# Optimization experiments

Hardware: AMD Instinct MI355X
Metric: run time of the kernel (lower is better)

Reference implementation:

```python
import jax, jax.numpy as jnp
import numpy as np

B, N, C = 8, 2000, 512
H, W, SR = 8, 5, 2          # num_heads, window_size, sr_ratio
LN_EPS = 1e-5


def setup_inputs() -> dict:
    key = jax.random.key(0)
    ks = jax.random.split(key, 6)
    s = lambda k, shape: jax.random.normal(k, shape, jnp.float32) * 0.02
    return {
        "x": jax.random.normal(ks[0], (B, N, C), jnp.float32),
        "Wq": s(ks[1], (C, C)),      "bq": jnp.zeros((C,), jnp.float32),
        "Wkv": s(ks[2], (2 * C, C)), "bkv": jnp.zeros((2 * C,), jnp.float32),
        "Wc": s(ks[3], (C, C)),      "bc": jnp.zeros((C,), jnp.float32),
        "ln_g": jnp.ones((C,), jnp.float32), "ln_b": jnp.zeros((C,), jnp.float32),
        "Wp": s(ks[4], (C, C)),      "bp": jnp.zeros((C,), jnp.float32),
    }


def reference(x, Wq, bq, Wkv, bkv, Wc, bc, ln_g, ln_b, Wp, bp):
    Bx, Nx, Cx = x.shape
    hd = Cx // H
    scale = hd ** (-0.5)
    G = Nx // W          # number of local windows
    M = Nx // SR         # pooled length

    # q: [B,H,N,hd]
    q = (x @ Wq.T + bq).reshape(Bx, Nx, H, hd).transpose(0, 2, 1, 3)

    # local kv: [B,G,W,2,H,hd] -> k_l/v_l [B,H,G,W,hd]
    kv = (x @ Wkv.T + bkv).reshape(Bx, G, W, 2, H, hd)
    k_l = kv[:, :, :, 0].transpose(0, 3, 1, 2, 4)
    v_l = kv[:, :, :, 1].transpose(0, 3, 1, 2, 4)

    # windowed local scores: group q into windows, einsum within window
    # (equivalent to torch's repeat_interleave + per-query matmul, but no blowup)
    qw = q.reshape(Bx, H, G, W, hd)
    attn_local = jnp.einsum('bhgqd,bhgkd->bhgqk', qw, k_l).reshape(Bx, H, Nx, W) * scale

    # pooled branch: AvgPool1d(sr) -> 1x1 conv -> LayerNorm -> GELU(exact)
    xp = x.reshape(Bx, M, SR, Cx).mean(axis=2)
    xp = xp @ Wc.T + bc
    mu = xp.mean(-1, keepdims=True)
    var = xp.var(-1, keepdims=True)
    xp = (xp - mu) / jnp.sqrt(var + LN_EPS) * ln_g + ln_b
    xp = jax.nn.gelu(xp, approximate=False)

    kvp = (xp @ Wkv.T + bkv).reshape(Bx, M, 2, H, hd)
    k_p = kvp[:, :, 0].transpose(0, 2, 1, 3)   # [B,H,M,hd]
    v_p = kvp[:, :, 1].transpose(0, 2, 1, 3)

    attn_pool = jnp.einsum('bhnd,bhmd->bhnm', q, k_p) * scale  # [B,H,N,M]

    # joint softmax over local window + pooled keys
    attn = jax.nn.softmax(jnp.concatenate([attn_local, attn_pool], axis=-1), axis=-1)
    a_l = attn[..., :W].reshape(Bx, H, G, W, W)
    a_p = attn[..., W:]

    x_l = jnp.einsum('bhgqk,bhgkd->bhgqd', a_l, v_l).reshape(Bx, H, Nx, hd)
    x_p = jnp.einsum('bhnm,bhmd->bhnd', a_p, v_p)

    out = (x_l + x_p).transpose(0, 2, 1, 3).reshape(Bx, Nx, Cx)
    return out @ Wp.T + bp
```

## Files before the change

### kernel.cpp

```cpp
#include <hip/hip_runtime.h>
#include <hip/hip_bf16.h>
#include <math.h>

#define B_   8
#define N_   2000
#define C_   512
#define H_   8
#define W_   5
#define SR_  2
#define M_   1000
#define HD_  64
#define KK_  512
#define RP_  8192
#define NPAD_ 16384
#define LN_EPS_ 1e-5f
#define SCALE_  0.125f
#define QSC_    0.18033688011112042f

#define TQ_   128
#define NCH_  16
#define KSTR2 72

typedef __attribute__((ext_vector_type(8))) short bf16x8;
typedef __attribute__((ext_vector_type(4))) short short4v;
typedef __attribute__((ext_vector_type(4))) float f32x4;
typedef __attribute__((ext_vector_type(16))) float f32x16;
#define MFMA16(a,b,c) __builtin_amdgcn_mfma_f32_16x16x32_bf16(a,b,c,0,0,0)
#define MFMA32(a,b,c) __builtin_amdgcn_mfma_f32_32x32x16_bf16(a,b,c,0,0,0)

__device__ __forceinline__ short f2bf(float f) {
  unsigned u = __float_as_uint(f);
  u += 0x7FFFu + ((u >> 16) & 1u);
  return (short)(u >> 16);
}
__device__ __forceinline__ uint2 pack4bf(float4 v) {
  unsigned a = ((unsigned)(unsigned short)f2bf(v.x)) | (((unsigned)(unsigned short)f2bf(v.y)) << 16);
  unsigned b = ((unsigned)(unsigned short)f2bf(v.z)) | (((unsigned)(unsigned short)f2bf(v.w)) << 16);
  return make_uint2(a, b);
}

__device__ __forceinline__ float wave_sum(float v) {
#pragma unroll
  for (int o = 32; o > 0; o >>= 1) v += __shfl_xor(v, o);
  return v;
}

__device__ __forceinline__ void gl_lds16(const void* g, void* l) {
  __builtin_amdgcn_global_load_lds(
      (const __attribute__((address_space(1))) void*)g,
      (__attribute__((address_space(3))) void*)l, 16, 0, 0);
}

__global__ __launch_bounds__(256) void cvt_bf16(const float* __restrict__ src,
                                                short* __restrict__ dst, int n8) {
  int i = blockIdx.x * 256 + threadIdx.x;
  if (i >= n8) return;
  float4 a = reinterpret_cast<const float4*>(src)[i * 2];
  float4 b = reinterpret_cast<const float4*>(src)[i * 2 + 1];
  uint2 pa = pack4bf(a), pb = pack4bf(b);
  reinterpret_cast<uint4*>(dst)[i] = make_uint4(pa.x, pa.y, pb.x, pb.y);
}

__global__ __launch_bounds__(256) void cvt_pool(const float* __restrict__ X,
                                                short* __restrict__ Xb,
                                                short* __restrict__ Xp) {
  int idx = blockIdx.x * 256 + threadIdx.x;
  const int total = B_ * M_ * (C_ / 8);
  if (idx >= total) return;
  int row = idx / (C_ / 8);
  int c8  = idx % (C_ / 8);
  int b = row / M_, m = row % M_;
  size_t r0 = ((size_t)b * N_ + 2 * m) * C_ + c8 * 8;
  size_t r1 = r0 + C_;
  float4 a0 = *(const float4*)(X + r0), a1 = *(const float4*)(X + r0 + 4);
  float4 b0 = *(const float4*)(X + r1), b1 = *(const float4*)(X + r1 + 4);
  uint2 pa0 = pack4bf(a0), pa1 = pack4bf(a1);
  uint2 pb0 = pack4bf(b0), pb1 = pack4bf(b1);
  *(uint4*)(Xb + r0) = make_uint4(pa0.x, pa0.y, pa1.x, pa1.y);
  *(uint4*)(Xb + r1) = make_uint4(pb0.x, pb0.y, pb1.x, pb1.y);
  float4 s0, s1;
  s0.x = 0.5f * (a0.x + b0.x); s0.y = 0.5f * (a0.y + b0.y);
  s0.z = 0.5f * (a0.z + b0.z); s0.w = 0.5f * (a0.w + b0.w);
  s1.x = 0.5f * (a1.x + b1.x); s1.y = 0.5f * (a1.y + b1.y);
  s1.z = 0.5f * (a1.z + b1.z); s1.w = 0.5f * (a1.w + b1.w);
  uint2 q0 = pack4bf(s0), q1 = pack4bf(s1);
  *(uint4*)(Xp + (size_t)row * C_ + c8 * 8) = make_uint4(q0.x, q0.y, q1.x, q1.y);
}

template<int OUT_BF16>
__global__ __launch_bounds__(256) void gemm_mfma(const short* __restrict__ A,
                                                 const short* __restrict__ Bm,
                                                 const float* __restrict__ bias,
                                                 void* __restrict__ Yv,
                                                 int O, float oscale) {
  __shared__ short As[128 * 32];
  __shared__ short Bs[128 * 32];
  const int tid  = threadIdx.x;
  const int w    = tid >> 6;
  const int lane = tid & 63;
  const int g    = lane >> 4;
  const int c0   = lane & 15;
  const int wr   = w >> 1;
  const int wc   = w & 1;
  const long r0 = (long)blockIdx.y * 128;
  const long o0 = (long)blockIdx.x * 128;
  const int srow = lane >> 2;
  const int scol = (lane & 3) * 8;

  f32x4 acc[4][4];
#pragma unroll
  for (int m = 0; m < 4; ++m)
#pragma unroll
    for (int n = 0; n < 4; ++n) acc[m][n] = (f32x4){0.f, 0.f, 0.f, 0.f};

  for (int kk = 0; kk < 16; ++kk) {
    __syncthreads();
#pragma unroll
    for (int i = 0; i < 2; ++i) {
      int arow = i * 64 + w * 16;
      gl_lds16(A  + (r0 + arow + srow) * KK_ + kk * 32 + scol, &As[arow * 32]);
      gl_lds16(Bm + (o0 + arow + srow) * KK_ + kk * 32 + scol, &Bs[arow * 32]);
    }
    __syncthreads();
    bf16x8 a[4], b[4];
#pragma unroll
    for (int m = 0; m < 4; ++m) a[m] = *(const bf16x8*)&As[(wr * 64 + m * 16 + c0) * 32 + g * 8];
#pragma unroll
    for (int n = 0; n < 4; ++n) b[n] = *(const bf16x8*)&Bs[(wc * 64 + n * 16 + c0) * 32 + g * 8];
#pragma unroll
    for (int m = 0; m < 4; ++m)
#pragma unroll
      for (int n = 0; n < 4; ++n) acc[m][n] = MFMA16(a[m], b[n], acc[m][n]);
  }

#pragma unroll
  for (int m = 0; m < 4; ++m) {
    long row = r0 + wr * 64 + m * 16 + g * 4;
#pragma unroll
    for (int n = 0; n < 4; ++n) {
      long col = o0 + wc * 64 + n * 16 + c0;
      float bv = bias[col];
#pragma unroll
      for (int r = 0; r < 4; ++r) {
        float v = (acc[m][n][r] + bv) * oscale;
        if (OUT_BF16) ((short*)Yv)[(row + r) * O + col] = f2bf(v);
        else          ((float*)Yv)[(row + r) * O + col] = v;
      }
    }
  }
}

__global__ __launch_bounds__(256) void gemm_qkv(const short* __restrict__ A,
                                                const short* __restrict__ Bm,
                                                const float* __restrict__ bq,
                                                const float* __restrict__ bkv,
                                                short* __restrict__ Yq,
                                                short* __restrict__ Ykv) {
  __shared__ short As[128 * 32];
  __shared__ short Bs[128 * 32];
  const int tid  = threadIdx.x;
  const int w    = tid >> 6;
  const int lane = tid & 63;
  const int g    = lane >> 4;
  const int c0   = lane & 15;
  const int wr   = w >> 1;
  const int wc   = w & 1;
  const long r0 = (long)blockIdx.y * 128;
  const long o0 = (long)blockIdx.x * 128;
  const int srow = lane >> 2;
  const int scol = (lane & 3) * 8;

  f32x4 acc[4][4];
#pragma unroll
  for (int m = 0; m < 4; ++m)
#pragma unroll
    for (int n = 0; n < 4; ++n) acc[m][n] = (f32x4){0.f, 0.f, 0.f, 0.f};

  for (int kk = 0; kk < 16; ++kk) {
    __syncthreads();
#pragma unroll
    for (int i = 0; i < 2; ++i) {
      int arow = i * 64 + w * 16;
      gl_lds16(A  + (r0 + arow + srow) * KK_ + kk * 32 + scol, &As[arow * 32]);
      gl_lds16(Bm + (o0 + arow + srow) * KK_ + kk * 32 + scol, &Bs[arow * 32]);
    }
    __syncthreads();
    bf16x8 a[4], b[4];
#pragma unroll
    for (int m = 0; m < 4; ++m) a[m] = *(const bf16x8*)&As[(wr * 64 + m * 16 + c0) * 32 + g * 8];
#pragma unroll
    for (int n = 0; n < 4; ++n) b[n] = *(const bf16x8*)&Bs[(wc * 64 + n * 16 + c0) * 32 + g * 8];
#pragma unroll
    for (int m = 0; m < 4; ++m)
#pragma unroll
      for (int n = 0; n < 4; ++n) acc[m][n] = MFMA16(a[m], b[n], acc[m][n]);
  }

  const bool isq = (blockIdx.x < 4);
#pragma unroll
  for (int m = 0; m < 4; ++m) {
    long row = r0 + wr * 64 + m * 16 + g * 4;
#pragma unroll
    for (int n = 0; n < 4; ++n) {
      long col = o0 + wc * 64 + n * 16 + c0;
      if (isq) {
        float bv = bq[col];
#pragma unroll
        for (int r = 0; r < 4; ++r)
          Yq[(row + r) * 512 + col] = f2bf((acc[m][n][r] + bv) * QSC_);
      } else {
        long ck = col - 512;
        float bv = bkv[ck];
#pragma unroll
        for (int r = 0; r < 4; ++r)
          Ykv[(row + r) * 1024 + ck] = f2bf(acc[m][n][r] + bv);
      }
    }
  }
}

__global__ __launch_bounds__(256) void ln_gelu(const float* __restrict__ Xc,
                                               short* __restrict__ Xo,
                                               const float* __restrict__ gam,
                                               const float* __restrict__ bet) {
  const int row = blockIdx.x;
  const float* p = Xc + (size_t)row * C_;
  const int t = threadIdx.x;
  float v0 = p[t], v1 = p[t + 256];
  float s  = wave_sum(v0 + v1);
  float ss = wave_sum(v0 * v0 + v1 * v1);
  __shared__ float rs[4], rss[4];
  const int w = t >> 6, lane = t & 63;
  if (lane == 0) { rs[w] = s; rss[w] = ss; }
  __syncthreads();
  float ts  = rs[0] + rs[1] + rs[2] + rs[3];
  float tss = rss[0] + rss[1] + rss[2] + rss[3];
  float mean = ts * (1.0f / C_);
  float var  = tss * (1.0f / C_) - mean * mean;
  float rstd = rsqrtf(var + LN_EPS_);
  float u0 = (v0 - mean) * rstd * gam[t]       + bet[t];
  float u1 = (v1 - mean) * rstd * gam[t + 256] + bet[t + 256];
  Xo[(size_t)row * C_ + t]       = f2bf(u0 * 0.5f * (1.0f + erff(u0 * 0.70710678118654752f)));
  Xo[(size_t)row * C_ + t + 256] = f2bf(u1 * 0.5f * (1.0f + erff(u1 * 0.70710678118654752f)));
}

template<int MODE>
__device__ __forceinline__ void tile32(const short* Ksb, const short* Vtb,
                                       const bf16x8 qf[4],
                                       float& m_c, float& l_c, f32x16* o,
                                       int c, int hi, int koff)
{
  f32x16 sblk[2];
  __builtin_amdgcn_s_setprio(1);
#pragma unroll
  for (int kb = 0; kb < 2; ++kb) {
    f32x16 acc = {};
#pragma unroll
    for (int sl = 0; sl < 4; ++sl) {
      bf16x8 kf = *(const bf16x8*)&Ksb[(kb*32 + c)*KSTR2 + sl*16 + hi*8];
      acc = MFMA32(kf, qf[sl], acc);
    }
    sblk[kb] = acc;
  }
  __builtin_amdgcn_s_setprio(0);

  if (MODE == 1) {
#pragma unroll
    for (int kb = 0; kb < 2; ++kb)
#pragma unroll
      for (int r = 0; r < 16; ++r) {
        int ku = koff + kb*32 + ((r & 3) + 8*(r >> 2));
        if ((unsigned)ku >= 5u) sblk[kb][r] = -3.0e38f;
      }
  }
  if (MODE == 2) {
#pragma unroll
    for (int r = 4; r < 16; ++r) sblk[1][r] = -3.0e38f;
  }

  float t16[16];
#pragma unroll
  for (int r = 0; r < 16; ++r) t16[r] = fmaxf(sblk[0][r], sblk[1][r]);
#pragma unroll
  for (int st = 8; st > 0; st >>= 1)
#pragma unroll
    for (int r = 0; r < st; ++r) t16[r] = fmaxf(t16[r], t16[r + st]);
  float pmax = fmaxf(t16[0], __shfl_xor(t16[0], 32));

  if (!__all(pmax - m_c <= 8.0f)) {
    float mn = fmaxf(m_c, pmax);
    float al = exp2f(m_c - mn);
    m_c = mn;
    l_c *= al;
    o[0] *= al;
    o[1] *= al;
  }

  float rs4[4] = {0.f, 0.f, 0.f, 0.f};
  int dw[2][8];
#pragma unroll
  for (int kb = 0; kb < 2; ++kb)
#pragma unroll
    for (int i = 0; i < 8; ++i) {
      float p0 = exp2f(sblk[kb][2*i]     - m_c);
      float p1 = exp2f(sblk[kb][2*i + 1] - m_c);
      rs4[i & 3] += p0 + p1;
      int d;
      asm("v_cvt_pk_bf16_f32 %0, %1, %2" : "=v"(d) : "v"(p0), "v"(p1));
      dw[kb][i] = d;
    }
  float rs = (rs4[0] + rs4[1]) + (rs4[2] + rs4[3]);
  rs += __shfl_xor(rs, 32);
  l_c += rs;

  bf16x8 pfrag[2][2];
#pragma unroll
  for (int kb = 0; kb < 2; ++kb)
#pragma unroll
    for (int kp = 0; kp < 2; ++kp) {
      union { int i[4]; bf16x8 v; } u;
      u.i[0] = dw[kb][kp*4 + 0];
      u.i[1] = dw[kb][kp*4 + 1];
      u.i[2] = dw[kb][kp*4 + 2];
      u.i[3] = dw[kb][kp*4 + 3];
      pfrag[kb][kp] = u.v;
    }

  __builtin_amdgcn_s_setprio(1);
#pragma unroll
  for (int db = 0; db < 2; ++db)
#pragma unroll
    for (int kb = 0; kb < 2; ++kb)
#pragma unroll
      for (int kp = 0; kp < 2; ++kp) {
        bf16x8 vf = *(const bf16x8*)&Vtb[(db*32 + c)*KSTR2 + kb*32 + kp*16 + hi*8];
        o[db] = MFMA32(vf, pfrag[kb][kp], o[db]);
      }
  __builtin_amdgcn_s_setprio(0);
}

__global__ __launch_bounds__(256, 3) void attn_mfma32(const short* __restrict__ Q,
                                                      const short* __restrict__ KV,
                                                      const short* __restrict__ KVP,
                                                      short* __restrict__ Oa) {
  __shared__ __align__(16) short Ks[2][64 * KSTR2];
  __shared__ __align__(16) short Vt[2][64 * KSTR2];

  const int bid   = blockIdx.x;
  const int bh    = bid & 63;
  const int chunk = bid >> 6;
  const int b     = bh >> 3;
  const int h     = bh & 7;
  const int n0    = chunk * TQ_;
  const int tid  = threadIdx.x;
  const int wq   = tid >> 6;
  const int lane = tid & 63;
  const int c    = lane & 31;
  const int hi   = lane >> 5;

  const int qabs = n0 + wq * 32 + c;
  const size_t qrow = (size_t)(b * N_ + qabs) * C_ + h * HD_;
  bf16x8 qf[4];
#pragma unroll
  for (int sl = 0; sl < 4; ++sl) qf[sl] = *(const bf16x8*)(Q + qrow + sl*16 + hi*8);

  const int qlo = (qabs / 5) * 5;
  const int klo = (n0 / 5) * 5;
  const int wlo = ((n0 + wq*32) / 5) * 5;
  const int whi = ((n0 + wq*32 + 31) / 5) * 5 + 5;

  const int kkey = tid >> 3, kdq = tid & 7;
  const int vkp  = tid & 31, vdq = (tid >> 5) & 7;
  const int svkp = (vkp & ~6) | ((vkp & 2) << 1) | ((vkp & 4) >> 1);
  bf16x8 rk0, rk1, rv0, rv1;

  auto issue = [&](const short* pb_) {
    rk0 = *(const bf16x8*)(pb_ + (size_t)kkey        * (2*C_) + h*HD_ + kdq*8);
    rk1 = *(const bf16x8*)(pb_ + (size_t)(kkey + 32) * (2*C_) + h*HD_ + kdq*8);
    rv0 = *(const bf16x8*)(pb_ + (size_t)(2*vkp)     * (2*C_) + C_ + h*HD_ + vdq*8);
    rv1 = *(const bf16x8*)(pb_ + (size_t)(2*vkp + 1) * (2*C_) + C_ + h*HD_ + vdq*8);
  };
  auto write = [&](int buf) {
    *(bf16x8*)&Ks[buf][kkey * KSTR2 + kdq * 8]        = rk0;
    *(bf16x8*)&Ks[buf][(kkey + 32) * KSTR2 + kdq * 8] = rk1;
#pragma unroll
    for (int e = 0; e < 8; ++e) {
      unsigned wv = ((unsigned)(unsigned short)rv0[e]) | (((unsigned)(unsigned short)rv1[e]) << 16);
      *(unsigned*)&Vt[buf][(vdq*8 + e) * KSTR2 + 2*svkp] = wv;
    }
  };

  const short* kvloc = KV  + (size_t)(b * N_ + klo) * (2*C_);
  const short* kvp_b = KVP + (size_t)(b * M_)       * (2*C_);

  float m_c = 0.f, l_c = 0.f;
  f32x16 o[2];
  o[0] = (f32x16){}; o[1] = (f32x16){};

  issue(kvloc);
  write(0);
  __syncthreads();
  int cur = 0;

#pragma unroll 1
  for (int t = 0; t < 3; ++t) {
    const short* nxt = (t < 2) ? kvloc + (size_t)(t + 1) * 64 * (2*C_) : kvp_b;
    issue(nxt);
    const int base = klo + t * 64;
    if (base < whi && base + 64 > wlo)
      tile32<1>(Ks[cur], Vt[cur], qf, m_c, l_c, o, c, hi, base + 4*hi - qlo);
    write(cur ^ 1);
    __syncthreads();
    cur ^= 1;
  }
#pragma unroll 1
  for (int t = 0; t < 15; ++t) {
    issue(kvp_b + (size_t)(t + 1) * 64 * (2*C_));
    tile32<0>(Ks[cur], Vt[cur], qf, m_c, l_c, o, c, hi, 0);
    write(cur ^ 1);
    __syncthreads();
    cur ^= 1;
  }
  tile32<2>(Ks[cur], Vt[cur], qf, m_c, l_c, o, c, hi, 0);

  if (qabs < N_) {
    float inv = 1.0f / l_c;
    short* orow = Oa + ((size_t)(b * N_ + qabs)) * C_ + h * HD_;
#pragma unroll
    for (int db = 0; db < 2; ++db)
#pragma unroll
      for (int rq = 0; rq < 4; ++rq) {
        short4v sv;
#pragma unroll
        for (int i = 0; i < 4; ++i) sv[i] = f2bf(o[db][rq*4 + i] * inv);
        *(short4v*)(orow + db*32 + rq*8 + 4*hi) = sv;
      }
  }
}

extern "C" void kernel_launch(void* const* d_in, const int* in_sizes, int n_in,
                              void* d_out, int out_size, void* d_ws, size_t ws_size,
                              hipStream_t stream) {
  const float* x   = (const float*)d_in[0];
  const float* Wq  = (const float*)d_in[1];
  const float* bq  = (const float*)d_in[2];
  const float* Wkv = (const float*)d_in[3];
  const float* bkv = (const float*)d_in[4];
  const float* Wc  = (const float*)d_in[5];
  const float* bc  = (const float*)d_in[6];
  const float* lng = (const float*)d_in[7];
  const float* lnb = (const float*)d_in[8];
  const float* Wp  = (const float*)d_in[9];
  const float* bp  = (const float*)d_in[10];
  float* out = (float*)d_out;

  float* xc   = (float*)d_ws;
  short* sb   = (short*)(xc + (size_t)RP_ * 512);
  short* xb    = sb;
  short* qb    = xb   + (size_t)16000 * 512;
  short* kvb   = qb   + (size_t)NPAD_ * 512;
  short* xpb   = kvb  + (size_t)NPAD_ * 1024;
  short* xcb   = xpb  + (size_t)RP_ * 512;
  short* kvpb  = xcb  + (size_t)RP_ * 512;
  short* aoutb = kvpb + (size_t)RP_ * 1024;
  short* Wqkvb = aoutb + (size_t)16000 * 512;
  short* Wcb   = Wqkvb + (size_t)1536 * 512;
  short* Wpb   = Wcb  + (size_t)512 * 512;

  dim3 blk(256);

  cvt_pool<<<dim3((B_*M_*(C_/8) + 255)/256), blk, 0, stream>>>(x, xb, xpb);
  cvt_bf16<<<dim3((512*512/8  + 255)/256), blk, 0, stream>>>(Wq,  Wqkvb,             512*512/8);
  cvt_bf16<<<dim3((1024*512/8 + 255)/256), blk, 0, stream>>>(Wkv, Wqkvb + 512*512,   1024*512/8);
  cvt_bf16<<<dim3((512*512/8  + 255)/256), blk, 0, stream>>>(Wc,  Wcb,  512*512/8);
  cvt_bf16<<<dim3((512*512/8  + 255)/256), blk, 0, stream>>>(Wp,  Wpb,  512*512/8);

  gemm_mfma<0><<<dim3(C_/128, RP_/128), blk, 0, stream>>>(xpb, Wcb, bc, xc, C_, 1.0f);
  ln_gelu<<<dim3(B_ * M_), blk, 0, stream>>>(xc, xcb, lng, lnb);
  gemm_mfma<1><<<dim3((2*C_)/128, RP_/128), blk, 0, stream>>>(xcb, Wqkvb + 512*512, bkv, kvpb, 2*C_, 1.0f);

  gemm_qkv<<<dim3(1536/128, 16000/128), blk, 0, stream>>>(xb, Wqkvb, bq, bkv, qb, kvb);

  attn_mfma32<<<dim3(64 * NCH_), blk, 0, stream>>>(qb, kvb, kvpb, aoutb);

  gemm_mfma<0><<<dim3(C_/128, 16000/128), blk, 0, stream>>>(aoutb, Wpb, bp, out, C_, 1.0f);
}
```

Measured before the change: 193.4 us.

## Double-buffer LDS tiles in both GEMM kernels and raise attention occupancy bound

Both the generic MFMA GEMM and the fused QKV GEMM now keep two LDS buffers per operand. The next K-slice is loaded with global-to-LDS copies while MFMAs run on the current slice, which leaves one barrier per iteration instead of two. The attention kernel's launch bounds are raised from 3 to 4 waves-per-EU minimum, which may force register spills in exchange for higher occupancy. LDS use per GEMM block doubles.

```diff
diff --git a/kernel.cpp b/kernel.cpp
--- a/kernel.cpp
+++ b/kernel.cpp
@@ -93,8 +93,8 @@
                                                  const float* __restrict__ bias,
                                                  void* __restrict__ Yv,
                                                  int O, float oscale) {
-  __shared__ short As[128 * 32];
-  __shared__ short Bs[128 * 32];
+  __shared__ short As[2][128 * 32];
+  __shared__ short Bs[2][128 * 32];
   const int tid  = threadIdx.x;
   const int w    = tid >> 6;
   const int lane = tid & 63;
@@ -107,30 +107,39 @@
   const int srow = lane >> 2;
   const int scol = (lane & 3) * 8;
 
-  f32x4 acc[4][4];
-#pragma unroll
-  for (int m = 0; m < 4; ++m)
-#pragma unroll
-    for (int n = 0; n < 4; ++n) acc[m][n] = (f32x4){0.f, 0.f, 0.f, 0.f};
-
-  for (int kk = 0; kk < 16; ++kk) {
-    __syncthreads();
+  auto stage = [&](int buf, int kk) {
 #pragma unroll
     for (int i = 0; i < 2; ++i) {
       int arow = i * 64 + w * 16;
-      gl_lds16(A  + (r0 + arow + srow) * KK_ + kk * 32 + scol, &As[arow * 32]);
-      gl_lds16(Bm + (o0 + arow + srow) * KK_ + kk * 32 + scol, &Bs[arow * 32]);
-    }
+      gl_lds16(A  + (r0 + arow + srow) * KK_ + kk * 32 + scol, &As[buf][arow * 32]);
+      gl_lds16(Bm + (o0 + arow + srow) * KK_ + kk * 32 + scol, &Bs[buf][arow * 32]);
+    }
+  };
+
+  f32x4 acc[4][4];
+#pragma unroll
+  for (int m = 0; m < 4; ++m)
+#pragma unroll
+    for (int n = 0; n < 4; ++n) acc[m][n] = (f32x4){0.f, 0.f, 0.f, 0.f};
+
+  stage(0, 0);
+  __syncthreads();
+  int cur = 0;
+
+#pragma unroll 1
+  for (int kk = 0; kk < 16; ++kk) {
+    if (kk < 15) stage(cur ^ 1, kk + 1);
+    bf16x8 a[4], b[4];
+#pragma unroll
+    for (int m = 0; m < 4; ++m) a[m] = *(const bf16x8*)&As[cur][(wr * 64 + m * 16 + c0) * 32 + g * 8];
+#pragma unroll
+    for (int n = 0; n < 4; ++n) b[n] = *(const bf16x8*)&Bs[cur][(wc * 64 + n * 16 + c0) * 32 + g * 8];
+#pragma unroll
+    for (int m = 0; m < 4; ++m)
+#pragma unroll
+      for (int n = 0; n < 4; ++n) acc[m][n] = MFMA16(a[m], b[n], acc[m][n]);
     __syncthreads();
-    bf16x8 a[4], b[4];
-#pragma unroll
-    for (int m = 0; m < 4; ++m) a[m] = *(const bf16x8*)&As[(wr * 64 + m * 16 + c0) * 32 + g * 8];
-#pragma unroll
-    for (int n = 0; n < 4; ++n) b[n] = *(const bf16x8*)&Bs[(wc * 64 + n * 16 + c0) * 32 + g * 8];
-#pragma unroll
-    for (int m = 0; m < 4; ++m)
-#pragma unroll
-      for (int n = 0; n < 4; ++n) acc[m][n] = MFMA16(a[m], b[n], acc[m][n]);
+    cur ^= 1;
   }
 
 #pragma unroll
@@ -156,8 +165,8 @@
                                                 const float* __restrict__ bkv,
                                                 short* __restrict__ Yq,
                                                 short* __restrict__ Ykv) {
-  __shared__ short As[128 * 32];
-  __shared__ short Bs[128 * 32];
+  __shared__ short As[2][128 * 32];
+  __shared__ short Bs[2][128 * 32];
   const int tid  = threadIdx.x;
   const int w    = tid >> 6;
   const int lane = tid & 63;
@@ -170,30 +179,39 @@
   const int srow = lane >> 2;
   const int scol = (lane & 3) * 8;
 
-  f32x4 acc[4][4];
-#pragma unroll
-  for (int m = 0; m < 4; ++m)
-#pragma unroll
-    for (int n = 0; n < 4; ++n) acc[m][n] = (f32x4){0.f, 0.f, 0.f, 0.f};
-
-  for (int kk = 0; kk < 16; ++kk) {
-    __syncthreads();
+  auto stage = [&](int buf, int kk) {
 #pragma unroll
     for (int i = 0; i < 2; ++i) {
       int arow = i * 64 + w * 16;
-      gl_lds16(A  + (r0 + arow + srow) * KK_ + kk * 32 + scol, &As[arow * 32]);
-      gl_lds16(Bm + (o0 + arow + srow) * KK_ + kk * 32 + scol, &Bs[arow * 32]);
-    }
+      gl_lds16(A  + (r0 + arow + srow) * KK_ + kk * 32 + scol, &As[buf][arow * 32]);
+      gl_lds16(Bm + (o0 + arow + srow) * KK_ + kk * 32 + scol, &Bs[buf][arow * 32]);
+    }
+  };
+
+  f32x4 acc[4][4];
+#pragma unroll
+  for (int m = 0; m < 4; ++m)
+#pragma unroll
+    for (int n = 0; n < 4; ++n) acc[m][n] = (f32x4){0.f, 0.f, 0.f, 0.f};
+
+  stage(0, 0);
+  __syncthreads();
+  int cur = 0;
+
+#pragma unroll 1
+  for (int kk = 0; kk < 16; ++kk) {
+    if (kk < 15) stage(cur ^ 1, kk + 1);
+    bf16x8 a[4], b[4];
+#pragma unroll
+    for (int m = 0; m < 4; ++m) a[m] = *(const bf16x8*)&As[cur][(wr * 64 + m * 16 + c0) * 32 + g * 8];
+#pragma unroll
+    for (int n = 0; n < 4; ++n) b[n] = *(const bf16x8*)&Bs[cur][(wc * 64 + n * 16 + c0) * 32 + g * 8];
+#pragma unroll
+    for (int m = 0; m < 4; ++m)
+#pragma unroll
+      for (int n = 0; n < 4; ++n) acc[m][n] = MFMA16(a[m], b[n], acc[m][n]);
     __syncthreads();
-    bf16x8 a[4], b[4];
-#pragma unroll
-    for (int m = 0; m < 4; ++m) a[m] = *(const bf16x8*)&As[(wr * 64 + m * 16 + c0) * 32 + g * 8];
-#pragma unroll
-    for (int n = 0; n < 4; ++n) b[n] = *(const bf16x8*)&Bs[(wc * 64 + n * 16 + c0) * 32 + g * 8];
-#pragma unroll
-    for (int m = 0; m < 4; ++m)
-#pragma unroll
-      for (int n = 0; n < 4; ++n) acc[m][n] = MFMA16(a[m], b[n], acc[m][n]);
+    cur ^= 1;
   }
 
   const bool isq = (blockIdx.x < 4);
@@ -339,7 +357,7 @@
   __builtin_amdgcn_s_setprio(0);
 }
 
-__global__ __launch_bounds__(256, 3) void attn_mfma32(const short* __restrict__ Q,
+__global__ __launch_bounds__(256, 4) void attn_mfma32(const short* __restrict__ Q,
                                                       const short* __restrict__ KV,
                                                       const short* __restrict__ KVP,
                                                       short* __restrict__ Oa) {
```

After: 195.3 us. No clear change (+1.0%).
